# Kernel optimization log

Measured on AMD Instinct MI355X. Metric: run time of the kernel, lower is better.

## Reference

```python
import jax, jax.numpy as jnp
import numpy as np

DIM = 128
B, LQ, LK = 8, 2048, 2048


def setup_inputs() -> dict:
    key = jax.random.key(0)
    k1, k2, k3 = jax.random.split(key, 3)
    output = jax.random.normal(k1, (B, LQ, DIM), dtype=jnp.float32)
    context = jax.random.normal(k2, (B, LK, DIM), dtype=jnp.float32)
    mask = jax.random.randint(k3, (B, LQ, LK), 0, 2).astype(jnp.bool_)
    return {"output": output, "context": context, "mask": mask}


def reference(output, context, mask):
    temperature = jnp.asarray(np.power(DIM, 0.5), dtype=output.dtype)
    # scores: [B, Lq, Lk]
    attn = jnp.einsum('bqd,bkd->bqk', output, context) / temperature
    attn = jnp.where(mask, -jnp.inf, attn)
    out_attn = jax.nn.log_softmax(attn, axis=-1)
    p = jax.nn.softmax(attn, axis=-1)
    # dropout is identity in eval/reference mode
    out = jnp.einsum('bqk,bkd->bqd', p, context)
    return (out, out_attn)
```

## Files before the change

### kernel.cpp

```cpp
#include <hip/hip_runtime.h>
#include <cstdint>


#define DIMV 128
constexpr int BB = 8;
constexpr int LQ = 2048;
constexpr int LK = 2048;
constexpr float QSCALE = 0.08838834764831843f;

typedef _Float16 half8 __attribute__((ext_vector_type(8)));
typedef _Float16 half4v __attribute__((ext_vector_type(4)));
typedef float float4v __attribute__((ext_vector_type(4)));

__global__ __launch_bounds__(256) void prep_kernel(const float* __restrict__ q,
                                                   const float* __restrict__ ctx,
                                                   _Float16* __restrict__ Qf,
                                                   _Float16* __restrict__ Kf,
                                                   _Float16* __restrict__ Vf) {
    __shared__ float tile[32][132];
    const int tid  = threadIdx.x;
    const int mode = blockIdx.x >> 9;
    const int t    = blockIdx.x & 511;
    const int b    = t >> 6;
    const int r0   = (t & 63) * 32;
    const float4* s4 = (const float4*)((mode == 0 ? q : ctx) + ((size_t)b * 2048 + r0) * DIMV);
    for (int v = 0; v < 4; v++) {
        int off = tid + v * 256;
        float4 f = s4[off];
        int row = off >> 5, c4 = (off & 31) * 4;
        tile[row][c4 + 0] = f.x; tile[row][c4 + 1] = f.y;
        tile[row][c4 + 2] = f.z; tile[row][c4 + 3] = f.w;
    }
    __syncthreads();
    if (mode < 2) {
        const float qs = (mode == 0) ? QSCALE : 1.0f;
        _Float16* dst = (mode == 0 ? Qf : Kf) + (size_t)b * (2048 * DIMV);
        for (int c = 0; c < 2; c++) {
            int chunk = tid + c * 256;
            int t2 = chunk >> 8, kk = (chunk >> 6) & 3, lane = chunk & 63;
            int quad = lane >> 4, l16 = lane & 15;
            int r = t2 * 16 + l16, d0 = kk * 32 + quad * 8;
            half8 h;
            for (int e = 0; e < 8; e++) h[e] = (_Float16)(tile[r][d0 + e] * qs);
            size_t tl = (size_t)(r0 >> 4) + t2;
            *(half8*)(dst + ((tl * 4 + kk) * 64 + lane) * 8) = h;
        }
    } else {
        _Float16* dst = Vf + (size_t)b * (2048 * DIMV);
        const int kt0 = r0 >> 4;
        for (int c = 0; c < 2; c++) {
            int chunk = tid + c * 256;
            int ktl = chunk >> 8, dp = (chunk >> 6) & 3, ln = chunk & 63;
            int qd = ln >> 4, s16 = ln & 15;
            half8 h;
            for (int e = 0; e < 4; e++) {
                h[e]     = (_Float16)tile[ktl * 16 + qd * 4 + e][(2 * dp) * 16 + s16];
                h[e + 4] = (_Float16)tile[ktl * 16 + qd * 4 + e][(2 * dp + 1) * 16 + s16];
            }
            *(half8*)(dst + ((((size_t)(kt0 + ktl)) * 4 + dp) * 64 + ln) * 8) = h;
        }
    }
}

__global__ __launch_bounds__(512, 2)
void attn_kernel(const unsigned char* __restrict__ mask,
                 const _Float16* __restrict__ Qf, const _Float16* __restrict__ Kf,
                 const _Float16* __restrict__ Vf,
                 float* __restrict__ out, float* __restrict__ out_attn) {
    __shared__ __attribute__((aligned(16))) float pvsum[2][32][132];
    __shared__ float redm[8][32], redl[8][32], swf[8][32];
    __shared__ float mcl32[32], rls32[32];

    const int tid  = threadIdx.x;
    const int wave = tid >> 6;
    const int lane = tid & 63;
    const int l16  = lane & 15;
    const int quad = lane >> 4;

    const int b  = blockIdx.x & 7;
    const int qg = blockIdx.x >> 3;
    const int q0 = qg * 32;

    const _Float16* Qb = Qf + (size_t)b * (2048 * DIMV);
    const _Float16* Kb = Kf + (size_t)b * (2048 * DIMV);
    const _Float16* Vb = Vf + (size_t)b * (2048 * DIMV);

    half8 qfrag[2][4];
#pragma unroll
    for (int sub = 0; sub < 2; sub++) {
        const size_t tq = (size_t)qg * 2 + sub;
#pragma unroll
        for (int kk = 0; kk < 4; kk++)
            qfrag[sub][kk] = *(const half8*)(Qb + ((tq * 4 + kk) * 64 + lane) * 8);
    }

    const unsigned char* mrow0 = mask + ((size_t)b * LQ + q0 + l16) * LK + wave * 256 + quad * 4;
    uint64_t mpack[2];
#pragma unroll
    for (int sub = 0; sub < 2; sub++) {
        uint64_t pk = 0;
#pragma unroll
        for (int ct = 0; ct < 16; ct++) {
            uint32_t w = *(const uint32_t*)(mrow0 + (size_t)sub * 16 * LK + ct * 16);
            w |= w >> 4; w |= w >> 2; w |= w >> 1;
            uint32_t nib = (w & 1u) | ((w >> 7) & 2u) | ((w >> 14) & 4u) | ((w >> 21) & 8u);
            pk |= (uint64_t)nib << (ct * 4);
        }
        mpack[sub] = pk;
    }

    const _Float16* kstrip = Kb + (size_t)wave * 16 * 2048;
    const _Float16* vstrip = Vb + (size_t)wave * 16 * 2048;

    const float NEGINF = -__builtin_inff();
    float m0r = -1e30f, m1r = -1e30f;
    float l0r = 0.f, l1r = 0.f;
    float4v oacc[2][8];
#pragma unroll
    for (int sub = 0; sub < 2; sub++)
#pragma unroll
        for (int dt = 0; dt < 8; dt++) oacc[sub][dt] = (float4v){0.f, 0.f, 0.f, 0.f};

    half8 kfb[2][4], vvb[2][4];
    {
#pragma unroll
        for (int kk = 0; kk < 4; kk++) kfb[0][kk] = *(const half8*)(kstrip + (kk * 64 + lane) * 8);
#pragma unroll
        for (int dp = 0; dp < 4; dp++) vvb[0][dp] = *(const half8*)(vstrip + (dp * 64 + lane) * 8);
    }

#pragma unroll 2
    for (int ct = 0; ct < 16; ++ct) {
        const int cur = ct & 1, nxt = cur ^ 1;
        const int cn  = (ct + 1) & 15;
        {
            const _Float16* kp = kstrip + (size_t)cn * 2048;
            const _Float16* vp = vstrip + (size_t)cn * 2048;
#pragma unroll
            for (int kk = 0; kk < 4; kk++) kfb[nxt][kk] = *(const half8*)(kp + (kk * 64 + lane) * 8);
#pragma unroll
            for (int dp = 0; dp < 4; dp++) vvb[nxt][dp] = *(const half8*)(vp + (dp * 64 + lane) * 8);
        }
        __builtin_amdgcn_sched_barrier(0);

#pragma unroll
        for (int sub = 0; sub < 2; sub++) {
            float4v st = (float4v){0.f, 0.f, 0.f, 0.f};
            __builtin_amdgcn_s_setprio(1);
#pragma unroll
            for (int kk = 0; kk < 4; kk++)
                st = __builtin_amdgcn_mfma_f32_16x16x32_f16(kfb[cur][kk], qfrag[sub][kk], st, 0, 0, 0);
            __builtin_amdgcn_s_setprio(0);
            const uint32_t mb = (uint32_t)(mpack[sub] >> (ct * 4)) & 0xFu;
            float& m = sub ? m1r : m0r;
            float& l = sub ? l1r : l0r;
            float sv[4];
#pragma unroll
            for (int r = 0; r < 4; r++) {
                float v = st[r];
                if ((mb >> r) & 1u) v = NEGINF;
                sv[r] = v;
            }
            float tmax = fmaxf(fmaxf(sv[0], sv[1]), fmaxf(sv[2], sv[3]));
            tmax = fmaxf(tmax, __shfl_xor(tmax, 16));
            tmax = fmaxf(tmax, __shfl_xor(tmax, 32));
            const bool upd = tmax > m + 3.0f;
            if (__any(upd)) {
                const float mnew = upd ? tmax : m;
                const float sc = __expf(m - mnew);
                float scr[4];
#pragma unroll
                for (int r = 0; r < 4; r++) scr[r] = __shfl(sc, quad * 4 + r);
                l *= sc;
#pragma unroll
                for (int dt = 0; dt < 8; dt++)
#pragma unroll
                    for (int r = 0; r < 4; r++) oacc[sub][dt][r] *= scr[r];
                m = mnew;
            }
            half4v pa;
            float pp[4];
#pragma unroll
            for (int r = 0; r < 4; r++) {
                pp[r] = __expf(sv[r] - m);
                pa[r] = (_Float16)pp[r];
            }
            __builtin_amdgcn_s_setprio(1);
#pragma unroll
            for (int dp = 0; dp < 4; dp++) {
                half4v vlo = __builtin_shufflevector(vvb[cur][dp], vvb[cur][dp], 0, 1, 2, 3);
                half4v vhi = __builtin_shufflevector(vvb[cur][dp], vvb[cur][dp], 4, 5, 6, 7);
                oacc[sub][2 * dp]     = __builtin_amdgcn_mfma_f32_16x16x16f16(pa, vlo, oacc[sub][2 * dp],     0, 0, 0);
                oacc[sub][2 * dp + 1] = __builtin_amdgcn_mfma_f32_16x16x16f16(pa, vhi, oacc[sub][2 * dp + 1], 0, 0, 0);
            }
            __builtin_amdgcn_s_setprio(0);
            float psum = (pp[0] + pp[1]) + (pp[2] + pp[3]);
            psum += __shfl_xor(psum, 16);
            psum += __shfl_xor(psum, 32);
            l += psum;
        }
    }

    if (quad == 0) {
        redm[wave][l16]      = m0r;  redm[wave][16 + l16] = m1r;
        redl[wave][l16]      = l0r;  redl[wave][16 + l16] = l1r;
    }
    half8 kf2[2][4];
#pragma unroll
    for (int kk = 0; kk < 4; kk++) kf2[0][kk] = *(const half8*)(kstrip + (kk * 64 + lane) * 8);
    __syncthreads();
    if (tid < 32) {
        float mm[8], ll[8];
#pragma unroll
        for (int p = 0; p < 8; p++) { mm[p] = redm[p][tid]; ll[p] = redl[p][tid]; }
        float M = mm[0];
#pragma unroll
        for (int p = 1; p < 8; p++) M = fmaxf(M, mm[p]);
        float L = 0.f;
#pragma unroll
        for (int p = 0; p < 8; p++) {
            const float e = __expf(mm[p] - M);
            swf[p][tid] = e;
            L += e * ll[p];
        }
        mcl32[tid] = M + __logf(L);
        rls32[tid] = 1.0f / L;
    }
    __syncthreads();

    for (int rnd = 0; rnd < 4; ++rnd) {
        if ((wave & 3) == rnd) {
            const int bf = wave >> 2;
#pragma unroll
            for (int sub = 0; sub < 2; sub++)
#pragma unroll
                for (int r = 0; r < 4; r++) {
                    const int row = sub * 16 + quad * 4 + r;
                    const float sc = swf[wave][row];
#pragma unroll
                    for (int dt = 0; dt < 8; dt++) {
                        const float v = oacc[sub][dt][r] * sc;
                        if (rnd == 0) pvsum[bf][row][dt * 16 + l16] = v;
                        else          pvsum[bf][row][dt * 16 + l16] += v;
                    }
                }
        }
        __syncthreads();
    }

    {
        const int row = tid >> 4;
        const int c0  = (tid & 15) * 8;
        const float rcl = rls32[row];
        float* op = out + ((size_t)b * LQ + q0 + row) * DIMV + c0;
#pragma unroll
        for (int h = 0; h < 2; h++) {
            float4v a0 = *(const float4v*)&pvsum[0][row][c0 + h * 4];
            float4v a1 = *(const float4v*)&pvsum[1][row][c0 + h * 4];
            float4v v;
#pragma unroll
            for (int j = 0; j < 4; j++) v[j] = (a0[j] + a1[j]) * rcl;
            *(float4v*)(op + h * 4) = v;
        }
    }

    const float mc0 = mcl32[l16];
    const float mc1 = mcl32[16 + l16];
    float* oa0 = out_attn + ((size_t)b * LQ + q0 + l16) * LK + wave * 256 + quad * 4;
#pragma unroll 2
    for (int ct = 0; ct < 16; ++ct) {
        const int cur = ct & 1, nxt = cur ^ 1;
        const int cn  = (ct + 1) & 15;
        {
            const _Float16* kp = kstrip + (size_t)cn * 2048;
#pragma unroll
            for (int kk = 0; kk < 4; kk++) kf2[nxt][kk] = *(const half8*)(kp + (kk * 64 + lane) * 8);
        }
        __builtin_amdgcn_sched_barrier(0);

#pragma unroll
        for (int sub = 0; sub < 2; sub++) {
            float4v st = (float4v){0.f, 0.f, 0.f, 0.f};
            __builtin_amdgcn_s_setprio(1);
#pragma unroll
            for (int kk = 0; kk < 4; kk++)
                st = __builtin_amdgcn_mfma_f32_16x16x32_f16(kf2[cur][kk], qfrag[sub][kk], st, 0, 0, 0);
            __builtin_amdgcn_s_setprio(0);
            const uint32_t mb = (uint32_t)(mpack[sub] >> (ct * 4)) & 0xFu;
            const float mc = sub ? mc1 : mc0;
            float4v o;
#pragma unroll
            for (int r = 0; r < 4; r++) {
                float lp = st[r] - mc;
                if ((mb >> r) & 1u) lp = -1.0e30f;
                o[r] = fmaxf(lp, -1.0e30f);
            }
            *(float4v*)(oa0 + (size_t)sub * 16 * LK + ct * 16) = o;
        }
    }
}

extern "C" void kernel_launch(void* const* d_in, const int* in_sizes, int n_in,
                              void* d_out, int out_size, void* d_ws, size_t ws_size,
                              hipStream_t stream) {
    const float* q_f32 = (const float*)d_in[0];
    const float* c_f32 = (const float*)d_in[1];
    const unsigned char* mask = (const unsigned char*)d_in[2];

    float* out      = (float*)d_out;
    float* out_attn = out + (size_t)BB * LQ * DIMV;

    _Float16* Qf = (_Float16*)d_ws;
    _Float16* Kf = Qf + (size_t)BB * LQ * DIMV;
    _Float16* Vf = Kf + (size_t)BB * LK * DIMV;

    prep_kernel<<<1536, 256, 0, stream>>>(q_f32, c_f32, Qf, Kf, Vf);
    attn_kernel<<<BB * (LQ / 32), 512, 0, stream>>>(mask, Qf, Kf, Vf, out, out_attn);
}
```

Measured before the change: 282.4 us.

## Cache scores in registers as fp16, use exact per-wave max, drop QK recompute

Each block now handles 16 query rows instead of 32, doubling the grid. Each wave computes its 16x256 score tile once, keeps it in registers as fp16, and takes the exact maximum before a separate PV pass. That removes the online-softmax rescaling and the second QK^T pass that previously recomputed scores to write log-probabilities, which are now produced from the cached fp16 scores. The cost is fp16 rounding in both the log-softmax output and the exponent input, more register pressure, and K/V being reloaded by twice as many blocks.

New measurement: 273.8 us. 1.03x faster.

```diff
diff --git a/kernel.cpp b/kernel.cpp
--- a/kernel.cpp
+++ b/kernel.cpp
@@ -51,11 +51,11 @@
         for (int c = 0; c < 2; c++) {
             int chunk = tid + c * 256;
             int ktl = chunk >> 8, dp = (chunk >> 6) & 3, ln = chunk & 63;
-            int qd = ln >> 4, s16 = ln & 15;
+            int qd = ln >> 4, s16i = ln & 15;
             half8 h;
             for (int e = 0; e < 4; e++) {
-                h[e]     = (_Float16)tile[ktl * 16 + qd * 4 + e][(2 * dp) * 16 + s16];
-                h[e + 4] = (_Float16)tile[ktl * 16 + qd * 4 + e][(2 * dp + 1) * 16 + s16];
+                h[e]     = (_Float16)tile[ktl * 16 + qd * 4 + e][(2 * dp) * 16 + s16i];
+                h[e + 4] = (_Float16)tile[ktl * 16 + qd * 4 + e][(2 * dp + 1) * 16 + s16i];
             }
             *(half8*)(dst + ((((size_t)(kt0 + ktl)) * 4 + dp) * 64 + ln) * 8) = h;
         }
@@ -67,9 +67,9 @@
                  const _Float16* __restrict__ Qf, const _Float16* __restrict__ Kf,
                  const _Float16* __restrict__ Vf,
                  float* __restrict__ out, float* __restrict__ out_attn) {
-    __shared__ __attribute__((aligned(16))) float pvsum[2][32][132];
-    __shared__ float redm[8][32], redl[8][32], swf[8][32];
-    __shared__ float mcl32[32], rls32[32];
+    __shared__ __attribute__((aligned(16))) float pvsum[2][16][132];
+    __shared__ float redm[8][16], redl[8][16], swf[8][16];
+    __shared__ float mcl16[16], rls16[16];
 
     const int tid  = threadIdx.x;
     const int wave = tid >> 6;
@@ -79,137 +79,111 @@
 
     const int b  = blockIdx.x & 7;
     const int qg = blockIdx.x >> 3;
-    const int q0 = qg * 32;
+    const int q0 = qg * 16;
 
     const _Float16* Qb = Qf + (size_t)b * (2048 * DIMV);
     const _Float16* Kb = Kf + (size_t)b * (2048 * DIMV);
     const _Float16* Vb = Vf + (size_t)b * (2048 * DIMV);
 
-    half8 qfrag[2][4];
-#pragma unroll
-    for (int sub = 0; sub < 2; sub++) {
-        const size_t tq = (size_t)qg * 2 + sub;
-#pragma unroll
-        for (int kk = 0; kk < 4; kk++)
-            qfrag[sub][kk] = *(const half8*)(Qb + ((tq * 4 + kk) * 64 + lane) * 8);
-    }
+    half8 qfrag[4];
+#pragma unroll
+    for (int kk = 0; kk < 4; kk++)
+        qfrag[kk] = *(const half8*)(Qb + (((size_t)qg * 4 + kk) * 64 + lane) * 8);
 
     const unsigned char* mrow0 = mask + ((size_t)b * LQ + q0 + l16) * LK + wave * 256 + quad * 4;
-    uint64_t mpack[2];
-#pragma unroll
-    for (int sub = 0; sub < 2; sub++) {
-        uint64_t pk = 0;
-#pragma unroll
-        for (int ct = 0; ct < 16; ct++) {
-            uint32_t w = *(const uint32_t*)(mrow0 + (size_t)sub * 16 * LK + ct * 16);
-            w |= w >> 4; w |= w >> 2; w |= w >> 1;
-            uint32_t nib = (w & 1u) | ((w >> 7) & 2u) | ((w >> 14) & 4u) | ((w >> 21) & 8u);
-            pk |= (uint64_t)nib << (ct * 4);
-        }
-        mpack[sub] = pk;
+    uint64_t mpack = 0;
+#pragma unroll
+    for (int ct = 0; ct < 16; ct++) {
+        uint32_t w = *(const uint32_t*)(mrow0 + ct * 16);
+        w |= w >> 4; w |= w >> 2; w |= w >> 1;
+        uint32_t nib = (w & 1u) | ((w >> 7) & 2u) | ((w >> 14) & 4u) | ((w >> 21) & 8u);
+        mpack |= (uint64_t)nib << (ct * 4);
     }
 
     const _Float16* kstrip = Kb + (size_t)wave * 16 * 2048;
     const _Float16* vstrip = Vb + (size_t)wave * 16 * 2048;
 
     const float NEGINF = -__builtin_inff();
-    float m0r = -1e30f, m1r = -1e30f;
-    float l0r = 0.f, l1r = 0.f;
-    float4v oacc[2][8];
-#pragma unroll
-    for (int sub = 0; sub < 2; sub++)
-#pragma unroll
-        for (int dt = 0; dt < 8; dt++) oacc[sub][dt] = (float4v){0.f, 0.f, 0.f, 0.f};
-
-    half8 kfb[2][4], vvb[2][4];
-    {
-#pragma unroll
-        for (int kk = 0; kk < 4; kk++) kfb[0][kk] = *(const half8*)(kstrip + (kk * 64 + lane) * 8);
-#pragma unroll
-        for (int dp = 0; dp < 4; dp++) vvb[0][dp] = *(const half8*)(vstrip + (dp * 64 + lane) * 8);
-    }
-
-#pragma unroll 2
+
+    half4v s16[16];
+    float smax = -3.0e38f;
+    half8 kfb[2][4];
+#pragma unroll
+    for (int kk = 0; kk < 4; kk++) kfb[0][kk] = *(const half8*)(kstrip + (kk * 64 + lane) * 8);
+
+#pragma unroll
     for (int ct = 0; ct < 16; ++ct) {
         const int cur = ct & 1, nxt = cur ^ 1;
-        const int cn  = (ct + 1) & 15;
-        {
-            const _Float16* kp = kstrip + (size_t)cn * 2048;
-            const _Float16* vp = vstrip + (size_t)cn * 2048;
+        if (ct < 15) {
+            const _Float16* kp = kstrip + (size_t)(ct + 1) * 2048;
 #pragma unroll
             for (int kk = 0; kk < 4; kk++) kfb[nxt][kk] = *(const half8*)(kp + (kk * 64 + lane) * 8);
+        }
+        __builtin_amdgcn_sched_barrier(0);
+        float4v st = (float4v){0.f, 0.f, 0.f, 0.f};
+        __builtin_amdgcn_s_setprio(1);
+#pragma unroll
+        for (int kk = 0; kk < 4; kk++)
+            st = __builtin_amdgcn_mfma_f32_16x16x32_f16(kfb[cur][kk], qfrag[kk], st, 0, 0, 0);
+        __builtin_amdgcn_s_setprio(0);
+        const uint32_t mb = (uint32_t)(mpack >> (ct * 4)) & 0xFu;
+        half4v h;
+        float sv[4];
+#pragma unroll
+        for (int r = 0; r < 4; r++) {
+            float v = st[r];
+            if ((mb >> r) & 1u) v = NEGINF;
+            sv[r] = v;
+            h[r] = (_Float16)v;
+        }
+        s16[ct] = h;
+        smax = fmaxf(smax, fmaxf(fmaxf(sv[0], sv[1]), fmaxf(sv[2], sv[3])));
+    }
+    smax = fmaxf(smax, __shfl_xor(smax, 16));
+    smax = fmaxf(smax, __shfl_xor(smax, 32));
+    const float m = fmaxf(smax, -1e30f);
+
+    float4v oacc[8];
+#pragma unroll
+    for (int dt = 0; dt < 8; dt++) oacc[dt] = (float4v){0.f, 0.f, 0.f, 0.f};
+    float ps = 0.f;
+    half8 vvb[2][4];
+#pragma unroll
+    for (int dp = 0; dp < 4; dp++) vvb[0][dp] = *(const half8*)(vstrip + (dp * 64 + lane) * 8);
+
+#pragma unroll
+    for (int ct = 0; ct < 16; ++ct) {
+        const int cur = ct & 1, nxt = cur ^ 1;
+        if (ct < 15) {
+            const _Float16* vp = vstrip + (size_t)(ct + 1) * 2048;
 #pragma unroll
             for (int dp = 0; dp < 4; dp++) vvb[nxt][dp] = *(const half8*)(vp + (dp * 64 + lane) * 8);
         }
         __builtin_amdgcn_sched_barrier(0);
-
-#pragma unroll
-        for (int sub = 0; sub < 2; sub++) {
-            float4v st = (float4v){0.f, 0.f, 0.f, 0.f};
-            __builtin_amdgcn_s_setprio(1);
-#pragma unroll
-            for (int kk = 0; kk < 4; kk++)
-                st = __builtin_amdgcn_mfma_f32_16x16x32_f16(kfb[cur][kk], qfrag[sub][kk], st, 0, 0, 0);
-            __builtin_amdgcn_s_setprio(0);
-            const uint32_t mb = (uint32_t)(mpack[sub] >> (ct * 4)) & 0xFu;
-            float& m = sub ? m1r : m0r;
-            float& l = sub ? l1r : l0r;
-            float sv[4];
-#pragma unroll
-            for (int r = 0; r < 4; r++) {
-                float v = st[r];
-                if ((mb >> r) & 1u) v = NEGINF;
-                sv[r] = v;
-            }
-            float tmax = fmaxf(fmaxf(sv[0], sv[1]), fmaxf(sv[2], sv[3]));
-            tmax = fmaxf(tmax, __shfl_xor(tmax, 16));
-            tmax = fmaxf(tmax, __shfl_xor(tmax, 32));
-            const bool upd = tmax > m + 3.0f;
-            if (__any(upd)) {
-                const float mnew = upd ? tmax : m;
-                const float sc = __expf(m - mnew);
-                float scr[4];
-#pragma unroll
-                for (int r = 0; r < 4; r++) scr[r] = __shfl(sc, quad * 4 + r);
-                l *= sc;
-#pragma unroll
-                for (int dt = 0; dt < 8; dt++)
-#pragma unroll
-                    for (int r = 0; r < 4; r++) oacc[sub][dt][r] *= scr[r];
-                m = mnew;
-            }
-            half4v pa;
-            float pp[4];
-#pragma unroll
-            for (int r = 0; r < 4; r++) {
-                pp[r] = __expf(sv[r] - m);
-                pa[r] = (_Float16)pp[r];
-            }
-            __builtin_amdgcn_s_setprio(1);
-#pragma unroll
-            for (int dp = 0; dp < 4; dp++) {
-                half4v vlo = __builtin_shufflevector(vvb[cur][dp], vvb[cur][dp], 0, 1, 2, 3);
-                half4v vhi = __builtin_shufflevector(vvb[cur][dp], vvb[cur][dp], 4, 5, 6, 7);
-                oacc[sub][2 * dp]     = __builtin_amdgcn_mfma_f32_16x16x16f16(pa, vlo, oacc[sub][2 * dp],     0, 0, 0);
-                oacc[sub][2 * dp + 1] = __builtin_amdgcn_mfma_f32_16x16x16f16(pa, vhi, oacc[sub][2 * dp + 1], 0, 0, 0);
-            }
-            __builtin_amdgcn_s_setprio(0);
-            float psum = (pp[0] + pp[1]) + (pp[2] + pp[3]);
-            psum += __shfl_xor(psum, 16);
-            psum += __shfl_xor(psum, 32);
-            l += psum;
-        }
-    }
-
-    if (quad == 0) {
-        redm[wave][l16]      = m0r;  redm[wave][16 + l16] = m1r;
-        redl[wave][l16]      = l0r;  redl[wave][16 + l16] = l1r;
-    }
-    half8 kf2[2][4];
-#pragma unroll
-    for (int kk = 0; kk < 4; kk++) kf2[0][kk] = *(const half8*)(kstrip + (kk * 64 + lane) * 8);
+        half4v pa;
+        float pp[4];
+#pragma unroll
+        for (int r = 0; r < 4; r++) {
+            pp[r] = __expf((float)s16[ct][r] - m);
+            pa[r] = (_Float16)pp[r];
+        }
+        __builtin_amdgcn_s_setprio(1);
+#pragma unroll
+        for (int dp = 0; dp < 4; dp++) {
+            half4v vlo = __builtin_shufflevector(vvb[cur][dp], vvb[cur][dp], 0, 1, 2, 3);
+            half4v vhi = __builtin_shufflevector(vvb[cur][dp], vvb[cur][dp], 4, 5, 6, 7);
+            oacc[2 * dp]     = __builtin_amdgcn_mfma_f32_16x16x16f16(pa, vlo, oacc[2 * dp],     0, 0, 0);
+            oacc[2 * dp + 1] = __builtin_amdgcn_mfma_f32_16x16x16f16(pa, vhi, oacc[2 * dp + 1], 0, 0, 0);
+        }
+        __builtin_amdgcn_s_setprio(0);
+        ps += (pp[0] + pp[1]) + (pp[2] + pp[3]);
+    }
+    ps += __shfl_xor(ps, 16);
+    ps += __shfl_xor(ps, 32);
+
+    if (quad == 0) { redm[wave][l16] = m; redl[wave][l16] = ps; }
     __syncthreads();
-    if (tid < 32) {
+    if (tid < 16) {
         float mm[8], ll[8];
 #pragma unroll
         for (int p = 0; p < 8; p++) { mm[p] = redm[p][tid]; ll[p] = redl[p][tid]; }
@@ -223,80 +197,54 @@
             swf[p][tid] = e;
             L += e * ll[p];
         }
-        mcl32[tid] = M + __logf(L);
-        rls32[tid] = 1.0f / L;
+        mcl16[tid] = M + __logf(L);
+        rls16[tid] = 1.0f / L;
     }
     __syncthreads();
+
+    {
+        const float mc = mcl16[l16];
+        float* oa0 = out_attn + ((size_t)b * LQ + q0 + l16) * LK + wave * 256 + quad * 4;
+#pragma unroll
+        for (int ct = 0; ct < 16; ++ct) {
+            float4v o;
+#pragma unroll
+            for (int r = 0; r < 4; r++) {
+                const float lp = (float)s16[ct][r] - mc;
+                o[r] = fmaxf(lp, -1.0e30f);
+            }
+            *(float4v*)(oa0 + ct * 16) = o;
+        }
+    }
 
     for (int rnd = 0; rnd < 4; ++rnd) {
         if ((wave & 3) == rnd) {
             const int bf = wave >> 2;
 #pragma unroll
-            for (int sub = 0; sub < 2; sub++)
-#pragma unroll
-                for (int r = 0; r < 4; r++) {
-                    const int row = sub * 16 + quad * 4 + r;
-                    const float sc = swf[wave][row];
-#pragma unroll
-                    for (int dt = 0; dt < 8; dt++) {
-                        const float v = oacc[sub][dt][r] * sc;
-                        if (rnd == 0) pvsum[bf][row][dt * 16 + l16] = v;
-                        else          pvsum[bf][row][dt * 16 + l16] += v;
-                    }
+            for (int r = 0; r < 4; r++) {
+                const int row = quad * 4 + r;
+                const float sc = swf[wave][row];
+#pragma unroll
+                for (int dt = 0; dt < 8; dt++) {
+                    const float v = oacc[dt][r] * sc;
+                    if (rnd == 0) pvsum[bf][row][dt * 16 + l16] = v;
+                    else          pvsum[bf][row][dt * 16 + l16] += v;
                 }
+            }
         }
         __syncthreads();
     }
 
     {
-        const int row = tid >> 4;
-        const int c0  = (tid & 15) * 8;
-        const float rcl = rls32[row];
-        float* op = out + ((size_t)b * LQ + q0 + row) * DIMV + c0;
-#pragma unroll
-        for (int h = 0; h < 2; h++) {
-            float4v a0 = *(const float4v*)&pvsum[0][row][c0 + h * 4];
-            float4v a1 = *(const float4v*)&pvsum[1][row][c0 + h * 4];
-            float4v v;
-#pragma unroll
-            for (int j = 0; j < 4; j++) v[j] = (a0[j] + a1[j]) * rcl;
-            *(float4v*)(op + h * 4) = v;
-        }
-    }
-
-    const float mc0 = mcl32[l16];
-    const float mc1 = mcl32[16 + l16];
-    float* oa0 = out_attn + ((size_t)b * LQ + q0 + l16) * LK + wave * 256 + quad * 4;
-#pragma unroll 2
-    for (int ct = 0; ct < 16; ++ct) {
-        const int cur = ct & 1, nxt = cur ^ 1;
-        const int cn  = (ct + 1) & 15;
-        {
-            const _Float16* kp = kstrip + (size_t)cn * 2048;
-#pragma unroll
-            for (int kk = 0; kk < 4; kk++) kf2[nxt][kk] = *(const half8*)(kp + (kk * 64 + lane) * 8);
-        }
-        __builtin_amdgcn_sched_barrier(0);
-
-#pragma unroll
-        for (int sub = 0; sub < 2; sub++) {
-            float4v st = (float4v){0.f, 0.f, 0.f, 0.f};
-            __builtin_amdgcn_s_setprio(1);
-#pragma unroll
-            for (int kk = 0; kk < 4; kk++)
-                st = __builtin_amdgcn_mfma_f32_16x16x32_f16(kf2[cur][kk], qfrag[sub][kk], st, 0, 0, 0);
-            __builtin_amdgcn_s_setprio(0);
-            const uint32_t mb = (uint32_t)(mpack[sub] >> (ct * 4)) & 0xFu;
-            const float mc = sub ? mc1 : mc0;
-            float4v o;
-#pragma unroll
-            for (int r = 0; r < 4; r++) {
-                float lp = st[r] - mc;
-                if ((mb >> r) & 1u) lp = -1.0e30f;
-                o[r] = fmaxf(lp, -1.0e30f);
-            }
-            *(float4v*)(oa0 + (size_t)sub * 16 * LK + ct * 16) = o;
-        }
+        const int row = tid >> 5;
+        const int c0  = (tid & 31) * 4;
+        const float rcl = rls16[row];
+        float4v a0 = *(const float4v*)&pvsum[0][row][c0];
+        float4v a1 = *(const float4v*)&pvsum[1][row][c0];
+        float4v v;
+#pragma unroll
+        for (int j = 0; j < 4; j++) v[j] = (a0[j] + a1[j]) * rcl;
+        *(float4v*)(out + ((size_t)b * LQ + q0 + row) * DIMV + c0) = v;
     }
 }
 
@@ -315,5 +263,5 @@
     _Float16* Vf = Kf + (size_t)BB * LK * DIMV;
 
     prep_kernel<<<1536, 256, 0, stream>>>(q_f32, c_f32, Qf, Kf, Vf);
-    attn_kernel<<<BB * (LQ / 32), 512, 0, stream>>>(mask, Qf, Kf, Vf, out, out_attn);
+    attn_kernel<<<BB * (LQ / 16), 512, 0, stream>>>(mask, Qf, Kf, Vf, out, out_attn);
 }
```
